# Kernel optimization log

Measured on AMD Instinct MI355X. Metric: run time of the kernel, lower is better.

Reference implementation:

```python
import jax, jax.numpy as jnp
import numpy as np
from jax import lax

# dims: batch, seq_len, d_model, heads, d_ff, num_scales, compression_ratio
B, L, D, H, F, S, CR = 4, 1024, 1024, 16, 4096, 4, 2


def setup_inputs() -> dict:
    key = jax.random.key(0)
    ks = jax.random.split(key, 12)
    def rn(k, shape, s=0.02):
        return jax.random.normal(k, shape, dtype=jnp.float32) * s
    return {
        'x': jax.random.normal(ks[0], (B, L, D), dtype=jnp.float32),
        'W_dc': rn(ks[1], (D, D, 3)),            # dilated conv kernel (OIH)
        'b_dc': jnp.zeros((D,), jnp.float32),
        'W_dec': rn(ks[2], (S - 1, D, D, CR)),    # strided decomposition convs
        'Wq': rn(ks[3], (S, D, D)),               # per-scale query proj
        'Wk': rn(ks[4], (S, D, D)),               # per-scale key proj
        'Wv': rn(ks[5], (D, D)),                  # shared value proj
        'Wo': rn(ks[6], (D, D)),                  # shared output proj
        'agg_logits': rn(ks[7], (S,), 1.0),       # convex aggregation logits
        'gamma1': jnp.ones((D,), jnp.float32), 'beta1': jnp.zeros((D,), jnp.float32),
        'gamma2': jnp.ones((D,), jnp.float32), 'beta2': jnp.zeros((D,), jnp.float32),
        'W1': rn(ks[8], (D, F)), 'b1': jnp.zeros((F,), jnp.float32),
        'W2': rn(ks[9], (F, D)), 'b2': jnp.zeros((D,), jnp.float32),
    }


def _conv1d(x_blc, w_oik, stride, pad, rdil):
    # x: [B, L, Cin] -> [B, L', Cout]; w: [Cout, Cin, K]
    y = lax.conv_general_dilated(
        x_blc.transpose(0, 2, 1), w_oik, (stride,), [(pad, pad)],
        rhs_dilation=(rdil,), dimension_numbers=('NCH', 'OIH', 'NCH'))
    return y.transpose(0, 2, 1)


def _ln(x, g, b, eps=1e-5):
    mu = x.mean(-1, keepdims=True)
    v = x.var(-1, keepdims=True)
    return (x - mu) * lax.rsqrt(v + eps) * g + b


def reference(x, W_dc, b_dc, W_dec, Wq, Wk, Wv, Wo, agg_logits,
              gamma1, beta1, gamma2, beta2, W1, b1, W2, b2):
    dh = D // H
    inv_sqrt_dh = 1.0 / jnp.sqrt(jnp.float32(dh))
    residual = x
    # 1. dilated conv (k=3, dil=2, pad=2 -> same length) + ReLU (dropout=eval/identity)
    xc = jax.nn.relu(_conv1d(x, W_dc, 1, 2, 2) + b_dc)
    # 2. hierarchical decomposition: strided convs halving seq length per scale
    scales = [xc]
    for s in range(S - 1):
        scales.append(_conv1d(scales[-1], W_dec[s], CR, 0, 1))
    # 3. multiscale attention: full-res queries attend to each compressed scale;
    #    value projection Wv shared across scales
    outs = []
    for s in range(S):
        Ls = scales[s].shape[1]
        q = (xc @ Wq[s]).reshape(B, L, H, dh)
        k = (scales[s] @ Wk[s]).reshape(B, Ls, H, dh)
        v = (scales[s] @ Wv).reshape(B, Ls, H, dh)
        att = jax.nn.softmax(jnp.einsum('bqhd,bkhd->bhqk', q, k) * inv_sqrt_dh, axis=-1)
        o = jnp.einsum('bhqk,bkhd->bqhd', att, v).reshape(B, L, D) @ Wo
        outs.append(o)
    # 4. convex (optimization-driven) aggregation + entropy sparsity aux loss
    w = jax.nn.softmax(agg_logits)
    maha = jnp.einsum('s,sbld->bld', w, jnp.stack(outs))
    aux_loss = -jnp.sum(w * jnp.log(w + 1e-9))
    # 5. residual + LN + FFN (exact GELU, as torch nn.GELU default)
    x1 = _ln(residual + maha, gamma1, beta1)
    ffn = jax.nn.gelu(x1 @ W1 + b1, approximate=False) @ W2 + b2
    out = _ln(x1 + ffn, gamma2, beta2)
    return out, aux_loss
```

## Files before the change

kernel.cpp:

```cpp
#include <hip/hip_runtime.h>
#include <cstddef>

#define DB 4
#define DL 1024
#define DD 1024
#define DH 16
#define DF 4096

typedef __attribute__((ext_vector_type(8))) short short8;
typedef __attribute__((ext_vector_type(4))) float float4v;

static __device__ __forceinline__ short f2bf(float f) {
    unsigned u = __float_as_uint(f);
    unsigned r = (u + 0x7FFFu + ((u >> 16) & 1u)) >> 16;
    return (short)r;
}

#define GLOAD_LDS16(gp, lp)                                                          \
    __builtin_amdgcn_global_load_lds(                                                \
        (const __attribute__((address_space(1))) void*)(gp),                         \
        (__attribute__((address_space(3))) void*)(lp), 16, 0, 0)

__global__ __launch_bounds__(256) void prep_all_kernel(
    const float* __restrict__ Wdc, const float* __restrict__ Wdec,
    const float* __restrict__ Wq, const float* __restrict__ Wk,
    const float* __restrict__ Wv, const float* __restrict__ Wo,
    const float* __restrict__ W1, const float* __restrict__ W2,
    const float* __restrict__ x, const float* __restrict__ agg,
    short* __restrict__ wdc_bt, short* __restrict__ wdec_bt,
    short* __restrict__ wq4t, short* __restrict__ wkvt, short* __restrict__ wot,
    short* __restrict__ w1t, short* __restrict__ w2t, short* __restrict__ xpad,
    float* __restrict__ wagg, float* __restrict__ aux) {
    __shared__ float tile[32][33];
    const size_t M1 = 1024 * 1024;
    int blk = blockIdx.x, tid = threadIdx.x;
    if (blk < 12288) {
        int idx = blk * 256 + tid;
        int i = idx & 1023, o = (idx >> 10) & 1023, k = idx >> 20;
        wdc_bt[idx] = f2bf(Wdc[((size_t)o * 1024 + i) * 3 + k]);
        return;
    }
    if (blk < 36864) {
        int idx = (blk - 12288) * 256 + tid;
        int i = idx & 1023, k2 = (idx >> 10) & 1, n = (idx >> 11) & 1023, s = idx >> 21;
        wdec_bt[idx] = f2bf(Wdec[(((size_t)(s * 1024 + n)) * 1024 + i) * 2 + k2]);
        return;
    }
    if (blk < 58368) {
        const float* src; short* dst; int K, N, bx, by;
        if (blk < 50176) {
            int r = blk - 36864;
            int z = r >> 10, rem = r & 1023;
            bx = rem & 31; by = rem >> 5; K = 1024; N = 1024;
            if (z < 4)      { src = Wq + (size_t)z * M1;       dst = wq4t + (size_t)z * M1; }
            else if (z < 8) { src = Wk + (size_t)(z - 4) * M1; dst = wkvt + (size_t)(z - 4) * 2 * M1; }
            else if (z < 12){ src = Wv;                        dst = wkvt + (size_t)(z - 8) * 2 * M1 + M1; }
            else            { src = Wo;                        dst = wot; }
        } else if (blk < 54272) {
            int r = blk - 50176;
            bx = r & 127; by = r >> 7; K = 1024; N = 4096; src = W1; dst = w1t;
        } else {
            int r = blk - 54272;
            bx = r & 31; by = r >> 5; K = 4096; N = 1024; src = W2; dst = w2t;
        }
        int n0 = bx << 5, k0 = by << 5;
        int cc = tid & 31, rr = tid >> 5;
#pragma unroll
        for (int p = 0; p < 4; p++) {
            int kk = (p << 3) + rr;
            tile[kk][cc] = src[(size_t)(k0 + kk) * N + n0 + cc];
        }
        __syncthreads();
#pragma unroll
        for (int p = 0; p < 4; p++) {
            int nn = (p << 3) + rr;
            dst[(size_t)(n0 + nn) * K + k0 + cc] = f2bf(tile[cc][nn]);
        }
        return;
    }
    if (blk < 74816) {
        int idx = (blk - 58368) * 256 + tid;
        int d = idx & 1023;
        int row = (idx >> 10) % 1028;
        int b = (idx >> 10) / 1028;
        int l = row - 2;
        float v = (l >= 0 && l < DL) ? x[((size_t)(b * DL + l)) * DD + d] : 0.f;
        xpad[idx] = f2bf(v);
        return;
    }
    if (tid == 0) {
        float l0 = agg[0], l1 = agg[1], l2 = agg[2], l3 = agg[3];
        float m = fmaxf(fmaxf(l0, l1), fmaxf(l2, l3));
        float e0 = __expf(l0 - m), e1 = __expf(l1 - m);
        float e2 = __expf(l2 - m), e3 = __expf(l3 - m);
        float ssum = e0 + e1 + e2 + e3;
        float w0 = e0 / ssum, w1 = e1 / ssum, w2 = e2 / ssum, w3 = e3 / ssum;
        wagg[0] = w0; wagg[1] = w1; wagg[2] = w2; wagg[3] = w3;
        *aux = -(w0 * logf(w0 + 1e-9f) + w1 * logf(w1 + 1e-9f) +
                 w2 * logf(w2 + 1e-9f) + w3 * logf(w3 + 1e-9f));
    }
}

template <int ACT, int OBF>
__global__ __launch_bounds__(256) void mgemm_kernel(
    const short* __restrict__ A, const short* __restrict__ Bt,
    const float* __restrict__ bias, void* __restrict__ Cv,
    int M, int N, int K) {
    __shared__ short As[128 * 32];
    __shared__ short Bs[128 * 32];
    int tid = threadIdx.x;
    int wave = tid >> 6, lane = tid & 63;
    int lq = lane & 15, quad = lane >> 4;
    int m0 = blockIdx.y << 7, n0 = blockIdx.x << 7;
    int wm = (wave & 1) << 6, wn = (wave >> 1) << 6;
    int r0 = tid >> 2, r1 = (256 + tid) >> 2;
    int kc0 = (tid & 3) << 3;
    const short* Ag0 = A + (size_t)(m0 + r0) * K + kc0;
    const short* Ag1 = A + (size_t)(m0 + r1) * K + kc0;
    const short* Bg0 = Bt + (size_t)(n0 + r0) * K + kc0;
    const short* Bg1 = Bt + (size_t)(n0 + r1) * K + kc0;
    float4v acc[4][4];
#pragma unroll
    for (int mi = 0; mi < 4; mi++)
#pragma unroll
        for (int ni = 0; ni < 4; ni++) acc[mi][ni] = (float4v){0.f, 0.f, 0.f, 0.f};

    for (int k0 = 0; k0 < K; k0 += 32) {
        __syncthreads();
        GLOAD_LDS16(Ag0 + k0, As + tid * 8);
        GLOAD_LDS16(Ag1 + k0, As + (256 + tid) * 8);
        GLOAD_LDS16(Bg0 + k0, Bs + tid * 8);
        GLOAD_LDS16(Bg1 + k0, Bs + (256 + tid) * 8);
        __syncthreads();
        short8 af[4], bfr[4];
#pragma unroll
        for (int mi = 0; mi < 4; mi++)
            af[mi] = *(const short8*)(As + ((wm + (mi << 4) + lq) << 5) + (quad << 3));
#pragma unroll
        for (int ni = 0; ni < 4; ni++)
            bfr[ni] = *(const short8*)(Bs + ((wn + (ni << 4) + lq) << 5) + (quad << 3));
#pragma unroll
        for (int mi = 0; mi < 4; mi++)
#pragma unroll
            for (int ni = 0; ni < 4; ni++)
                acc[mi][ni] = __builtin_amdgcn_mfma_f32_16x16x32_bf16(
                    af[mi], bfr[ni], acc[mi][ni], 0, 0, 0);
    }
#pragma unroll
    for (int ni = 0; ni < 4; ni++) {
        int col = n0 + wn + (ni << 4) + lq;
        float bv = bias ? bias[col] : 0.f;
#pragma unroll
        for (int mi = 0; mi < 4; mi++) {
#pragma unroll
            for (int r = 0; r < 4; r++) {
                int row = m0 + wm + (mi << 4) + (quad << 2) + r;
                float v = acc[mi][ni][r] + bv;
                if (ACT == 1) v = 0.5f * v * (1.0f + erff(v * 0.70710678118654752f));
                if (OBF) ((short*)Cv)[(size_t)row * N + col] = f2bf(v);
                else ((float*)Cv)[(size_t)row * N + col] = v;
            }
        }
    }
}

__global__ __launch_bounds__(256) void kvgemm_kernel(
    const short* __restrict__ acts, const short* __restrict__ wkvt,
    short* __restrict__ kvall, short* __restrict__ kfrall) {
    __shared__ short As[128 * 32];
    __shared__ short Bs[128 * 32];
    int my = blockIdx.y;
    int s = my < 32 ? 0 : my < 48 ? 1 : my < 56 ? 2 : 3;
    int m0 = my << 7;
    int rb = s == 0 ? 0 : s == 1 ? 4096 : s == 2 ? 6144 : 7168;
    size_t doff = s == 0 ? 0 : s == 1 ? 4194304 : s == 2 ? 6291456 : 7340032;
    int Ls = DL >> s;
    const short* Bt = wkvt + (size_t)s * 2097152;
    const int K = 1024, N = 2048;
    int tid = threadIdx.x;
    int wave = tid >> 6, lane = tid & 63;
    int lq = lane & 15, quad = lane >> 4;
    int n0 = blockIdx.x << 7;
    int wm = (wave & 1) << 6, wn = (wave >> 1) << 6;
    int r0 = tid >> 2, r1 = (256 + tid) >> 2;
    int kc0 = (tid & 3) << 3;
    const short* Ag0 = acts + (size_t)(m0 + r0) * K + kc0;
    const short* Ag1 = acts + (size_t)(m0 + r1) * K + kc0;
    const short* Bg0 = Bt + (size_t)(n0 + r0) * K + kc0;
    const short* Bg1 = Bt + (size_t)(n0 + r1) * K + kc0;
    float4v acc[4][4];
#pragma unroll
    for (int mi = 0; mi < 4; mi++)
#pragma unroll
        for (int ni = 0; ni < 4; ni++) acc[mi][ni] = (float4v){0.f, 0.f, 0.f, 0.f};
    for (int k0 = 0; k0 < K; k0 += 32) {
        __syncthreads();
        GLOAD_LDS16(Ag0 + k0, As + tid * 8);
        GLOAD_LDS16(Ag1 + k0, As + (256 + tid) * 8);
        GLOAD_LDS16(Bg0 + k0, Bs + tid * 8);
        GLOAD_LDS16(Bg1 + k0, Bs + (256 + tid) * 8);
        __syncthreads();
        short8 af[4], bfr[4];
#pragma unroll
        for (int mi = 0; mi < 4; mi++)
            af[mi] = *(const short8*)(As + ((wm + (mi << 4) + lq) << 5) + (quad << 3));
#pragma unroll
        for (int ni = 0; ni < 4; ni++)
            bfr[ni] = *(const short8*)(Bs + ((wn + (ni << 4) + lq) << 5) + (quad << 3));
#pragma unroll
        for (int mi = 0; mi < 4; mi++)
#pragma unroll
            for (int ni = 0; ni < 4; ni++)
                acc[mi][ni] = __builtin_amdgcn_mfma_f32_16x16x32_bf16(
                    af[mi], bfr[ni], acc[mi][ni], 0, 0, 0);
    }
    bool isK = (n0 < 1024);
#pragma unroll
    for (int ni = 0; ni < 4; ni++) {
        int col = n0 + wn + (ni << 4) + lq;
        if (isK) {
            int h = col >> 6, dc = (col >> 3) & 7, di = col & 7;
#pragma unroll
            for (int mi = 0; mi < 4; mi++)
#pragma unroll
                for (int r = 0; r < 4; r++) {
                    int row = m0 + wm + (mi << 4) + (quad << 2) + r;
                    int jg = row - rb;
                    int b = jg >> (10 - s);
                    int j = jg & (Ls - 1);
                    int bh = (b << 4) | h;
                    size_t addr = doff + (((size_t)bh * (Ls >> 4) + (j >> 4)) << 10) +
                                  (dc << 7) + ((j & 15) << 3) + di;
                    kfrall[addr] = f2bf(acc[mi][ni][r]);
                }
        } else {
#pragma unroll
            for (int mi = 0; mi < 4; mi++)
#pragma unroll
                for (int r = 0; r < 4; r++) {
                    int row = m0 + wm + (mi << 4) + (quad << 2) + r;
                    kvall[(size_t)row * N + col] = f2bf(acc[mi][ni][r]);
                }
        }
    }
}

__global__ __launch_bounds__(256) void mgemm_pk_kernel(
    const short* __restrict__ A, const short* __restrict__ Bt,
    const float* __restrict__ bias, float* __restrict__ Cout,
    int M, int N, int Kfull, int KH) {
    __shared__ short As[128 * 32];
    __shared__ short Bs[128 * 32];
    int kz = blockIdx.z;
    const short* Ab = A + (size_t)kz * KH;
    const short* Btb = Bt + (size_t)kz * KH;
    float* Co = Cout + (size_t)kz * M * N;
    int tid = threadIdx.x;
    int wave = tid >> 6, lane = tid & 63;
    int lq = lane & 15, quad = lane >> 4;
    int m0 = blockIdx.y << 7, n0 = blockIdx.x << 7;
    int wm = (wave & 1) << 6, wn = (wave >> 1) << 6;
    int r0 = tid >> 2, r1 = (256 + tid) >> 2;
    int kc0 = (tid & 3) << 3;
    const short* Ag0 = Ab + (size_t)(m0 + r0) * Kfull + kc0;
    const short* Ag1 = Ab + (size_t)(m0 + r1) * Kfull + kc0;
    const short* Bg0 = Btb + (size_t)(n0 + r0) * Kfull + kc0;
    const short* Bg1 = Btb + (size_t)(n0 + r1) * Kfull + kc0;
    float4v acc[4][4];
#pragma unroll
    for (int mi = 0; mi < 4; mi++)
#pragma unroll
        for (int ni = 0; ni < 4; ni++) acc[mi][ni] = (float4v){0.f, 0.f, 0.f, 0.f};
    for (int k0 = 0; k0 < KH; k0 += 32) {
        __syncthreads();
        GLOAD_LDS16(Ag0 + k0, As + tid * 8);
        GLOAD_LDS16(Ag1 + k0, As + (256 + tid) * 8);
        GLOAD_LDS16(Bg0 + k0, Bs + tid * 8);
        GLOAD_LDS16(Bg1 + k0, Bs + (256 + tid) * 8);
        __syncthreads();
        short8 af[4], bfr[4];
#pragma unroll
        for (int mi = 0; mi < 4; mi++)
            af[mi] = *(const short8*)(As + ((wm + (mi << 4) + lq) << 5) + (quad << 3));
#pragma unroll
        for (int ni = 0; ni < 4; ni++)
            bfr[ni] = *(const short8*)(Bs + ((wn + (ni << 4) + lq) << 5) + (quad << 3));
#pragma unroll
        for (int mi = 0; mi < 4; mi++)
#pragma unroll
            for (int ni = 0; ni < 4; ni++)
                acc[mi][ni] = __builtin_amdgcn_mfma_f32_16x16x32_bf16(
                    af[mi], bfr[ni], acc[mi][ni], 0, 0, 0);
    }
#pragma unroll
    for (int ni = 0; ni < 4; ni++) {
        int col = n0 + wn + (ni << 4) + lq;
        float bv = (bias && kz == 0) ? bias[col] : 0.f;
#pragma unroll
        for (int mi = 0; mi < 4; mi++)
#pragma unroll
            for (int r = 0; r < 4; r++) {
                int row = m0 + wm + (mi << 4) + (quad << 2) + r;
                __builtin_nontemporal_store(acc[mi][ni][r] + bv,
                                            &Co[(size_t)row * N + col]);
            }
    }
}

__global__ __launch_bounds__(256) void sumcast4_kernel(
    const float* __restrict__ p, size_t stride, short* __restrict__ outp) {
    int idx = (blockIdx.x * 256 + threadIdx.x) << 2;
    float4v a0 = __builtin_nontemporal_load((const float4v*)&p[idx]);
    float4v a1 = __builtin_nontemporal_load((const float4v*)&p[stride + idx]);
    float4v a2 = __builtin_nontemporal_load((const float4v*)&p[2 * stride + idx]);
    float4v a3 = __builtin_nontemporal_load((const float4v*)&p[3 * stride + idx]);
    ushort4 u;
    u.x = (unsigned short)f2bf(a0[0] + a1[0] + a2[0] + a3[0]);
    u.y = (unsigned short)f2bf(a0[1] + a1[1] + a2[1] + a3[1]);
    u.z = (unsigned short)f2bf(a0[2] + a1[2] + a2[2] + a3[2]);
    u.w = (unsigned short)f2bf(a0[3] + a1[3] + a2[3] + a3[3]);
    *(ushort4*)&outp[idx] = u;
}

__global__ __launch_bounds__(256) void convdil_pk_kernel(
    const short* __restrict__ xp, const short* __restrict__ Wt,
    float* __restrict__ pbuf) {
    __shared__ short As[128 * 32];
    __shared__ short Bs[128 * 32];
    int kp = blockIdx.z;
    int tid = threadIdx.x;
    int wave = tid >> 6, lane = tid & 63;
    int lq = lane & 15, quad = lane >> 4;
    int m0 = blockIdx.y << 7, n0 = blockIdx.x << 7;
    int wm = (wave & 1) << 6, wn = (wave >> 1) << 6;
    int b = m0 >> 10, ll0 = m0 & 1023;
    int r0 = tid >> 2, r1 = (256 + tid) >> 2;
    int kc = (tid & 3) << 3;
    float* Co = pbuf + (size_t)kp * DB * DL * DD;
    const short* Abase = xp + ((size_t)(b * 1028 + ll0 + 2 * kp)) * DD + kc;
    const short* Bbase = Wt + (size_t)kp * DD * DD;
    const short* Bg0 = Bbase + (size_t)(n0 + r0) * DD + kc;
    const short* Bg1 = Bbase + (size_t)(n0 + r1) * DD + kc;
    float4v acc[4][4];
#pragma unroll
    for (int mi = 0; mi < 4; mi++)
#pragma unroll
        for (int ni = 0; ni < 4; ni++) acc[mi][ni] = (float4v){0.f, 0.f, 0.f, 0.f};
    for (int k0 = 0; k0 < DD; k0 += 32) {
        __syncthreads();
        GLOAD_LDS16(Abase + (size_t)r0 * DD + k0, As + tid * 8);
        GLOAD_LDS16(Abase + (size_t)r1 * DD + k0, As + (256 + tid) * 8);
        GLOAD_LDS16(Bg0 + k0, Bs + tid * 8);
        GLOAD_LDS16(Bg1 + k0, Bs + (256 + tid) * 8);
        __syncthreads();
        short8 af[4], bfr[4];
#pragma unroll
        for (int mi = 0; mi < 4; mi++)
            af[mi] = *(const short8*)(As + ((wm + (mi << 4) + lq) << 5) + (quad << 3));
#pragma unroll
        for (int ni = 0; ni < 4; ni++)
            bfr[ni] = *(const short8*)(Bs + ((wn + (ni << 4) + lq) << 5) + (quad << 3));
#pragma unroll
        for (int mi = 0; mi < 4; mi++)
#pragma unroll
            for (int ni = 0; ni < 4; ni++)
                acc[mi][ni] = __builtin_amdgcn_mfma_f32_16x16x32_bf16(
                    af[mi], bfr[ni], acc[mi][ni], 0, 0, 0);
    }
#pragma unroll
    for (int ni = 0; ni < 4; ni++) {
        int col = n0 + wn + (ni << 4) + lq;
#pragma unroll
        for (int mi = 0; mi < 4; mi++)
#pragma unroll
            for (int r = 0; r < 4; r++) {
                int row = m0 + wm + (mi << 4) + (quad << 2) + r;
                __builtin_nontemporal_store(acc[mi][ni][r],
                                            &Co[(size_t)row * DD + col]);
            }
    }
}

__global__ __launch_bounds__(256) void convcomb_kernel(
    const float* __restrict__ pbuf, const float* __restrict__ bvec,
    short* __restrict__ xcb) {
    const size_t M4 = (size_t)DB * DL * DD;
    int idx = (blockIdx.x * 256 + threadIdx.x) << 2;
    int col = idx & 1023;
    float4v p0 = __builtin_nontemporal_load((const float4v*)&pbuf[idx]);
    float4v p1 = __builtin_nontemporal_load((const float4v*)&pbuf[M4 + idx]);
    float4v p2 = __builtin_nontemporal_load((const float4v*)&pbuf[2 * M4 + idx]);
    float4v bb = *(const float4v*)&bvec[col];
    ushort4 u;
    u.x = (unsigned short)f2bf(fmaxf(p0[0] + p1[0] + p2[0] + bb[0], 0.f));
    u.y = (unsigned short)f2bf(fmaxf(p0[1] + p1[1] + p2[1] + bb[1], 0.f));
    u.z = (unsigned short)f2bf(fmaxf(p0[2] + p1[2] + p2[2] + bb[2], 0.f));
    u.w = (unsigned short)f2bf(fmaxf(p0[3] + p1[3] + p2[3] + bb[3], 0.f));
    *(ushort4*)&xcb[idx] = u;
}

__global__ __launch_bounds__(256) void vfrag_all_kernel(const short* __restrict__ kvall,
                                                        short* __restrict__ vfr0) {
    __shared__ short tile[32][33];
    int flat = blockIdx.x;
    int s, base, rb;
    size_t doff;
    if (flat < 4096)      { s = 0; base = 0;    rb = 0;    doff = 0; }
    else if (flat < 6144) { s = 1; base = 4096; rb = 4096; doff = 4194304; }
    else if (flat < 7168) { s = 2; base = 6144; rb = 6144; doff = 6291456; }
    else                  { s = 3; base = 7168; rb = 7168; doff = 7340032; }
    int rem = flat - base;
    int Ls = DL >> s;
    int nt = Ls >> 5;
    int j0t = rem & (nt - 1);
    int rest = rem >> (5 - s);
    int dt = rest & 1;
    int bh = rest >> 1;
    int j0 = j0t << 5, d0 = dt << 5;
    int b = bh >> 4, h = bh & 15;
    int tid = threadIdx.x;
    int cc = tid & 31, rr = tid >> 5;
#pragma unroll
    for (int p = 0; p < 4; p++) {
        int jj = (p << 3) + rr;
        tile[jj][cc] = kvall[((size_t)(rb + b * Ls + j0 + jj) << 11) + 1024 +
                             (h << 6) + d0 + cc];
    }
    __syncthreads();
    int c = j0 >> 6, ks = (j0 >> 5) & 1;
    int pc = (((cc >> 2) & 1) << 4) | ((cc >> 3) << 2) | (cc & 3);
#pragma unroll
    for (int p = 0; p < 4; p++) {
        int d = d0 + (p << 3) + rr;
        int tt = d >> 4, lqv = d & 15;
        size_t off = doff + (((size_t)bh * (Ls >> 6) + c) << 12) + (ks << 11) +
                     (tt << 9) + ((cc & 24) << 4) + (lqv << 3) + (cc & 7);
        vfr0[off] = tile[pc][(p << 3) + rr];
    }
}

static __device__ __forceinline__ float fexp2(float x) {
    return __builtin_amdgcn_exp2f(x);
}

#define STAGE9(BUF, TILE)                                                         \
    {                                                                             \
        const short* _gs = (w < 2)                                                \
            ? kt + ((size_t)(TILE) << 12) + (w << 11) + (lane << 3)               \
            : vt + ((size_t)(TILE) << 12) + ((w - 2) << 11) + (lane << 3);        \
        short* _lb = sbuf[BUF] + (w << 11) + (lane << 3);                         \
        _Pragma("unroll") for (int _i = 0; _i < 4; _i++)                          \
            GLOAD_LDS16(_gs + (_i << 9), _lb + (_i << 9));                        \
    }

__global__ __launch_bounds__(256) void attn_fused9_kernel(
    const short* __restrict__ qb4, const short* __restrict__ kfr0,
    const short* __restrict__ vfr0, const float* __restrict__ wagg,
    short* __restrict__ attb) {
    __shared__ __align__(16) short sbuf[2][8192];
    int tid = threadIdx.x;
    int w = tid >> 6, lane = tid & 63;
    int lq = lane & 15, quad = lane >> 4;
    int bh = blockIdx.x;
    int b = bh >> 4, h = bh & 15;
    int qrow0 = b * DL + (blockIdx.y << 6) + (w << 4);
    const float c_exp = 0.18033688f;
    int fo = (quad << 7) + (lq << 3);

    float fin[4][4];
#pragma unroll
    for (int t = 0; t < 4; t++)
#pragma unroll
        for (int r = 0; r < 4; r++) fin[t][r] = 0.f;

#pragma unroll 1
    for (int s = 0; s < 4; s++) {
        int Ls = DL >> s;
        size_t doff = s == 0 ? 0 : s == 1 ? 4194304 : s == 2 ? 6291456 : 7340032;

        const short* qbase = qb4 + ((size_t)(qrow0 + lq) << 12) + (s << 10) +
                             (h << 6) + (quad << 3);
        short8 qf0 = __builtin_nontemporal_load((const short8*)qbase);
        short8 qf1 = __builtin_nontemporal_load((const short8*)(qbase + 32));

        const short* kt = kfr0 + doff + (((size_t)bh * (Ls >> 4)) << 10);
        const short* vt = vfr0 + doff + (((size_t)bh * (Ls >> 6)) << 12);

        float4v O[4];
        float lsum = 0.f;
#pragma unroll
        for (int t = 0; t < 4; t++) O[t] = (float4v){0.f, 0.f, 0.f, 0.f};

        int nt = Ls >> 6;
        STAGE9(0, 0);
#pragma unroll 1
        for (int c = 0; c < nt; c++) {
            __syncthreads();
            int cur = c & 1;
            if (c + 1 < nt) STAGE9(cur ^ 1, c + 1);
            const short* kl = sbuf[cur] + fo;
            const short* vl = sbuf[cur] + 4096 + fo;

            float4v S[4];
#pragma unroll
            for (int t = 0; t < 4; t++) {
                short8 kf0 = *(const short8*)(kl + (t << 10));
                short8 kf1 = *(const short8*)(kl + (t << 10) + 512);
                float4v zz = (float4v){0.f, 0.f, 0.f, 0.f};
                zz = __builtin_amdgcn_mfma_f32_16x16x32_bf16(kf0, qf0, zz, 0, 0, 0);
                S[t] = __builtin_amdgcn_mfma_f32_16x16x32_bf16(kf1, qf1, zz, 0, 0, 0);
            }

            unsigned wpk[8];
#pragma unroll
            for (int t = 0; t < 4; t++) {
                float p0 = fexp2(S[t][0] * c_exp);
                float p1 = fexp2(S[t][1] * c_exp);
                float p2 = fexp2(S[t][2] * c_exp);
                float p3 = fexp2(S[t][3] * c_exp);
                lsum += p0 + p1 + p2 + p3;
                wpk[2 * t]     = (__float_as_uint(p1) & 0xFFFF0000u) |
                                 (__float_as_uint(p0) >> 16);
                wpk[2 * t + 1] = (__float_as_uint(p3) & 0xFFFF0000u) |
                                 (__float_as_uint(p2) >> 16);
            }
            union AFU { unsigned u[4]; short8 s8; };
            AFU af0, af1;
            af0.u[0] = wpk[0]; af0.u[1] = wpk[1]; af0.u[2] = wpk[2]; af0.u[3] = wpk[3];
            af1.u[0] = wpk[4]; af1.u[1] = wpk[5]; af1.u[2] = wpk[6]; af1.u[3] = wpk[7];
#pragma unroll
            for (int t = 0; t < 4; t++) {
                short8 vf = *(const short8*)(vl + (t << 9));
                O[t] = __builtin_amdgcn_mfma_f32_16x16x32_bf16(af0.s8, vf, O[t], 0, 0, 0);
            }
#pragma unroll
            for (int t = 0; t < 4; t++) {
                short8 vf = *(const short8*)(vl + 2048 + (t << 9));
                O[t] = __builtin_amdgcn_mfma_f32_16x16x32_bf16(af1.s8, vf, O[t], 0, 0, 0);
            }
        }
        __syncthreads();

        lsum += __shfl_xor(lsum, 16, 64);
        lsum += __shfl_xor(lsum, 32, 64);
        float wsc = wagg[s];
#pragma unroll
        for (int r = 0; r < 4; r++) {
            int sl = (lane & 48) | (((lane >> 4) << 2) + r);
            float lr = __shfl(lsum, sl, 64);
            float linv = wsc / lr;
#pragma unroll
            for (int t = 0; t < 4; t++) fin[t][r] += O[t][r] * linv;
        }
    }
#pragma unroll
    for (int r = 0; r < 4; r++) {
        size_t rbase = ((size_t)(qrow0 + (quad << 2) + r) << 10) + (h << 6) + lq;
#pragma unroll
        for (int t = 0; t < 4; t++)
            attb[rbase + (t << 4)] = f2bf(fin[t][r]);
    }
}

template <int NP, int OBF>
__global__ __launch_bounds__(256) void addlnN_kernel(
    const float* __restrict__ a, const float* __restrict__ pb, size_t pstride,
    const float* __restrict__ gam, const float* __restrict__ bet,
    float* __restrict__ out, short* __restrict__ outb) {
    __shared__ float redA[4], redB[4];
    int row = blockIdx.x, tid = threadIdx.x;
    size_t base = (size_t)row * DD + (tid << 2);
    float4v av = *(const float4v*)&a[base];
    float s0 = av[0], s1 = av[1], s2 = av[2], s3 = av[3];
#pragma unroll
    for (int j = 0; j < NP; j++) {
        float4v pv = __builtin_nontemporal_load(
            (const float4v*)&pb[(size_t)j * pstride + base]);
        s0 += pv[0]; s1 += pv[1]; s2 += pv[2]; s3 += pv[3];
    }
    float lsum = s0 + s1 + s2 + s3;
    float lsq = s0 * s0 + s1 * s1 + s2 * s2 + s3 * s3;
#pragma unroll
    for (int o = 32; o > 0; o >>= 1) {
        lsum += __shfl_down(lsum, o, 64);
        lsq += __shfl_down(lsq, o, 64);
    }
    int lane = tid & 63, wid = tid >> 6;
    if (lane == 0) { redA[wid] = lsum; redB[wid] = lsq; }
    __syncthreads();
    float tsum = redA[0] + redA[1] + redA[2] + redA[3];
    float tsq = redB[0] + redB[1] + redB[2] + redB[3];
    float mean = tsum * (1.0f / DD);
    float var = tsq * (1.0f / DD) - mean * mean;
    float rstd = rsqrtf(var + 1e-5f);
    float4v gv = *(const float4v*)&gam[tid << 2];
    float4v bev = *(const float4v*)&bet[tid << 2];
    float4v o;
    o[0] = (s0 - mean) * rstd * gv[0] + bev[0];
    o[1] = (s1 - mean) * rstd * gv[1] + bev[1];
    o[2] = (s2 - mean) * rstd * gv[2] + bev[2];
    o[3] = (s3 - mean) * rstd * gv[3] + bev[3];
    *(float4v*)&out[base] = o;
    if (OBF) {
        ushort4 u;
        u.x = (unsigned short)f2bf(o[0]);
        u.y = (unsigned short)f2bf(o[1]);
        u.z = (unsigned short)f2bf(o[2]);
        u.w = (unsigned short)f2bf(o[3]);
        *(ushort4*)&outb[base] = u;
    }
}

extern "C" void kernel_launch(void* const* d_in, const int* in_sizes, int n_in,
                              void* d_out, int out_size, void* d_ws, size_t ws_size,
                              hipStream_t stream) {
    (void)in_sizes; (void)n_in; (void)out_size; (void)ws_size;
    const float* x   = (const float*)d_in[0];
    const float* Wdc = (const float*)d_in[1];
    const float* bdc = (const float*)d_in[2];
    const float* Wdec= (const float*)d_in[3];
    const float* Wq  = (const float*)d_in[4];
    const float* Wk  = (const float*)d_in[5];
    const float* Wv  = (const float*)d_in[6];
    const float* Wo  = (const float*)d_in[7];
    const float* agg = (const float*)d_in[8];
    const float* g1  = (const float*)d_in[9];
    const float* be1 = (const float*)d_in[10];
    const float* g2  = (const float*)d_in[11];
    const float* be2 = (const float*)d_in[12];
    const float* W1  = (const float*)d_in[13];
    const float* b1  = (const float*)d_in[14];
    const float* W2  = (const float*)d_in[15];
    const float* b2  = (const float*)d_in[16];
    float* out = (float*)d_out;

    float* ws = (float*)d_ws;
    size_t off = 0;
    auto alloc = [&](size_t nfloats) { float* p = ws + off; off += nfloats; return p; };
    const size_t M1 = 1024 * 1024;
    short* wdc_bt  = (short*)alloc(3 * M1 / 2);
    short* wdec_bt = (short*)alloc(3 * M1);
    short* wq4t    = (short*)alloc(2 * M1);
    short* wkvt    = (short*)alloc(4 * M1);
    short* wot     = (short*)alloc(M1 / 2);
    short* w1t     = (short*)alloc(2 * M1);
    short* w2t     = (short*)alloc(2 * M1);
    float* wagg    = alloc(64);
    short* xpad    = (short*)alloc(2105344);
    short* xcb     = (short*)alloc(2 * M1);
    short* s1b     = (short*)alloc(M1);
    short* s2b     = (short*)alloc(M1 / 2);
    short* s3b     = (short*)alloc(M1 / 4);
    short* qb4     = (short*)alloc(8 * M1);
    short* kvall   = (short*)alloc(7 * M1 + M1 / 2);
    short* kfrall  = (short*)alloc(3 * M1 + 3 * M1 / 4);
    short* vfrall  = (short*)alloc(3 * M1 + 3 * M1 / 4);
    short* attb    = (short*)alloc(2 * M1);
    float* x1      = alloc(4 * M1);
    short* x1b     = (short*)alloc(2 * M1);
    float* pkbuf   = alloc(8 * M1);
    short* hb      = qb4;
    float* convp   = (float*)qb4;
    float* pk4     = (float*)kvall;

    dim3 blk(256);
    prep_all_kernel<<<dim3(74817), blk, 0, stream>>>(
        Wdc, Wdec, Wq, Wk, Wv, Wo, W1, W2, x, agg,
        wdc_bt, wdec_bt, wq4t, wkvt, wot, w1t, w2t, xpad, wagg,
        out + (size_t)DB * DL * DD);

    convdil_pk_kernel<<<dim3(DD / 128, DB * DL / 128, 3), blk, 0, stream>>>(
        xpad, wdc_bt, convp);
    convcomb_kernel<<<dim3(4 * M1 / (256 * 4)), blk, 0, stream>>>(convp, bdc, xcb);

    mgemm_pk_kernel<<<dim3(8, 16, 4), blk, 0, stream>>>(
        xcb, wdec_bt, nullptr, pkbuf, 2048, DD, 2 * DD, 512);
    sumcast4_kernel<<<dim3(2 * M1 / 1024), blk, 0, stream>>>(pkbuf, 2 * M1, s1b);
    mgemm_pk_kernel<<<dim3(8, 8, 4), blk, 0, stream>>>(
        s1b, wdec_bt + 2 * M1, nullptr, pkbuf, 1024, DD, 2 * DD, 512);
    sumcast4_kernel<<<dim3(M1 / 1024), blk, 0, stream>>>(pkbuf, M1, s2b);
    mgemm_pk_kernel<<<dim3(8, 4, 4), blk, 0, stream>>>(
        s2b, wdec_bt + 4 * M1, nullptr, pkbuf, 512, DD, 2 * DD, 512);
    sumcast4_kernel<<<dim3(M1 / 2048), blk, 0, stream>>>(pkbuf, M1 / 2, s3b);

    mgemm_kernel<0, 1><<<dim3(32, 32), blk, 0, stream>>>(
        xcb, wq4t, nullptr, qb4, DB * DL, 4 * DD, DD);

    kvgemm_kernel<<<dim3(16, 60), blk, 0, stream>>>(xcb, wkvt, kvall, kfrall);

    vfrag_all_kernel<<<dim3(7680), blk, 0, stream>>>(kvall, vfrall);

    attn_fused9_kernel<<<dim3(DB * DH, DL / 64), blk, 0, stream>>>(
        qb4, kfrall, vfrall, wagg, attb);

    mgemm_pk_kernel<<<dim3(8, 32, 2), blk, 0, stream>>>(
        attb, wot, nullptr, pkbuf, DB * DL, DD, DD, DD / 2);

    addlnN_kernel<2, 1><<<dim3(DB * DL), blk, 0, stream>>>(
        x, pkbuf, 4 * M1, g1, be1, x1, x1b);

    mgemm_kernel<1, 1><<<dim3(DF / 128, (DB * DL) / 128), blk, 0, stream>>>(
        x1b, w1t, b1, hb, DB * DL, DF, DD);
    mgemm_pk_kernel<<<dim3(8, 32, 4), blk, 0, stream>>>(
        hb, w2t, b2, pk4, DB * DL, DD, DF, DF / 4);

    addlnN_kernel<4, 0><<<dim3(DB * DL), blk, 0, stream>>>(
        x1, pk4, 4 * M1, g2, be2, out, nullptr);
}
```

Before: 700.8 us.

## Double-buffer LDS tiles in all MFMA GEMM kernels to overlap loads with compute

Each of the four bf16 MFMA GEMM kernels (generic, KV projection, split-K, dilated conv) now keeps two LDS buffers for the A and B tiles. The next K-tile's global-to-LDS loads are issued before the MFMAs on the current tile, and a single barrier per iteration replaces the previous two. The aim is to hide global memory latency behind matrix-core work and cut barrier overhead. In exchange, LDS use per block doubles to 32 KB, which may lower occupancy. The benefit also depends on whether the barrier forces a full vmcnt wait.

```diff
diff --git a/kernel.cpp b/kernel.cpp
--- a/kernel.cpp
+++ b/kernel.cpp
@@ -106,8 +106,8 @@
     const short* __restrict__ A, const short* __restrict__ Bt,
     const float* __restrict__ bias, void* __restrict__ Cv,
     int M, int N, int K) {
-    __shared__ short As[128 * 32];
-    __shared__ short Bs[128 * 32];
+    __shared__ short As[2][128 * 32];
+    __shared__ short Bs[2][128 * 32];
     int tid = threadIdx.x;
     int wave = tid >> 6, lane = tid & 63;
     int lq = lane & 15, quad = lane >> 4;
@@ -125,27 +125,35 @@
 #pragma unroll
         for (int ni = 0; ni < 4; ni++) acc[mi][ni] = (float4v){0.f, 0.f, 0.f, 0.f};
 
-    for (int k0 = 0; k0 < K; k0 += 32) {
-        __syncthreads();
-        GLOAD_LDS16(Ag0 + k0, As + tid * 8);
-        GLOAD_LDS16(Ag1 + k0, As + (256 + tid) * 8);
-        GLOAD_LDS16(Bg0 + k0, Bs + tid * 8);
-        GLOAD_LDS16(Bg1 + k0, Bs + (256 + tid) * 8);
-        __syncthreads();
+#define MG_STAGE(BUF, KO)                                                \
+    {                                                                    \
+        GLOAD_LDS16(Ag0 + (KO), As[BUF] + tid * 8);                      \
+        GLOAD_LDS16(Ag1 + (KO), As[BUF] + (256 + tid) * 8);              \
+        GLOAD_LDS16(Bg0 + (KO), Bs[BUF] + tid * 8);                      \
+        GLOAD_LDS16(Bg1 + (KO), Bs[BUF] + (256 + tid) * 8);              \
+    }
+    int nk = K >> 5;
+    MG_STAGE(0, 0);
+    __syncthreads();
+    for (int t = 0; t < nk; t++) {
+        int cur = t & 1;
+        if (t + 1 < nk) MG_STAGE(cur ^ 1, (t + 1) << 5);
         short8 af[4], bfr[4];
 #pragma unroll
         for (int mi = 0; mi < 4; mi++)
-            af[mi] = *(const short8*)(As + ((wm + (mi << 4) + lq) << 5) + (quad << 3));
+            af[mi] = *(const short8*)(As[cur] + ((wm + (mi << 4) + lq) << 5) + (quad << 3));
 #pragma unroll
         for (int ni = 0; ni < 4; ni++)
-            bfr[ni] = *(const short8*)(Bs + ((wn + (ni << 4) + lq) << 5) + (quad << 3));
+            bfr[ni] = *(const short8*)(Bs[cur] + ((wn + (ni << 4) + lq) << 5) + (quad << 3));
 #pragma unroll
         for (int mi = 0; mi < 4; mi++)
 #pragma unroll
             for (int ni = 0; ni < 4; ni++)
                 acc[mi][ni] = __builtin_amdgcn_mfma_f32_16x16x32_bf16(
                     af[mi], bfr[ni], acc[mi][ni], 0, 0, 0);
-    }
+        __syncthreads();
+    }
+#undef MG_STAGE
 #pragma unroll
     for (int ni = 0; ni < 4; ni++) {
         int col = n0 + wn + (ni << 4) + lq;
@@ -167,8 +175,8 @@
 __global__ __launch_bounds__(256) void kvgemm_kernel(
     const short* __restrict__ acts, const short* __restrict__ wkvt,
     short* __restrict__ kvall, short* __restrict__ kfrall) {
-    __shared__ short As[128 * 32];
-    __shared__ short Bs[128 * 32];
+    __shared__ short As[2][128 * 32];
+    __shared__ short Bs[2][128 * 32];
     int my = blockIdx.y;
     int s = my < 32 ? 0 : my < 48 ? 1 : my < 56 ? 2 : 3;
     int m0 = my << 7;
@@ -193,27 +201,36 @@
     for (int mi = 0; mi < 4; mi++)
 #pragma unroll
         for (int ni = 0; ni < 4; ni++) acc[mi][ni] = (float4v){0.f, 0.f, 0.f, 0.f};
-    for (int k0 = 0; k0 < K; k0 += 32) {
-        __syncthreads();
-        GLOAD_LDS16(Ag0 + k0, As + tid * 8);
-        GLOAD_LDS16(Ag1 + k0, As + (256 + tid) * 8);
-        GLOAD_LDS16(Bg0 + k0, Bs + tid * 8);
-        GLOAD_LDS16(Bg1 + k0, Bs + (256 + tid) * 8);
-        __syncthreads();
+
+#define KV_STAGE(BUF, KO)                                                \
+    {                                                                    \
+        GLOAD_LDS16(Ag0 + (KO), As[BUF] + tid * 8);                      \
+        GLOAD_LDS16(Ag1 + (KO), As[BUF] + (256 + tid) * 8);              \
+        GLOAD_LDS16(Bg0 + (KO), Bs[BUF] + tid * 8);                      \
+        GLOAD_LDS16(Bg1 + (KO), Bs[BUF] + (256 + tid) * 8);              \
+    }
+    int nk = K >> 5;
+    KV_STAGE(0, 0);
+    __syncthreads();
+    for (int t = 0; t < nk; t++) {
+        int cur = t & 1;
+        if (t + 1 < nk) KV_STAGE(cur ^ 1, (t + 1) << 5);
         short8 af[4], bfr[4];
 #pragma unroll
         for (int mi = 0; mi < 4; mi++)
-            af[mi] = *(const short8*)(As + ((wm + (mi << 4) + lq) << 5) + (quad << 3));
+            af[mi] = *(const short8*)(As[cur] + ((wm + (mi << 4) + lq) << 5) + (quad << 3));
 #pragma unroll
         for (int ni = 0; ni < 4; ni++)
-            bfr[ni] = *(const short8*)(Bs + ((wn + (ni << 4) + lq) << 5) + (quad << 3));
+            bfr[ni] = *(const short8*)(Bs[cur] + ((wn + (ni << 4) + lq) << 5) + (quad << 3));
 #pragma unroll
         for (int mi = 0; mi < 4; mi++)
 #pragma unroll
             for (int ni = 0; ni < 4; ni++)
                 acc[mi][ni] = __builtin_amdgcn_mfma_f32_16x16x32_bf16(
                     af[mi], bfr[ni], acc[mi][ni], 0, 0, 0);
-    }
+        __syncthreads();
+    }
+#undef KV_STAGE
     bool isK = (n0 < 1024);
 #pragma unroll
     for (int ni = 0; ni < 4; ni++) {
@@ -249,8 +266,8 @@
     const short* __restrict__ A, const short* __restrict__ Bt,
     const float* __restrict__ bias, float* __restrict__ Cout,
     int M, int N, int Kfull, int KH) {
-    __shared__ short As[128 * 32];
-    __shared__ short Bs[128 * 32];
+    __shared__ short As[2][128 * 32];
+    __shared__ short Bs[2][128 * 32];
     int kz = blockIdx.z;
     const short* Ab = A + (size_t)kz * KH;
     const short* Btb = Bt + (size_t)kz * KH;
@@ -271,27 +288,36 @@
     for (int mi = 0; mi < 4; mi++)
 #pragma unroll
         for (int ni = 0; ni < 4; ni++) acc[mi][ni] = (float4v){0.f, 0.f, 0.f, 0.f};
-    for (int k0 = 0; k0 < KH; k0 += 32) {
-        __syncthreads();
-        GLOAD_LDS16(Ag0 + k0, As + tid * 8);
-        GLOAD_LDS16(Ag1 + k0, As + (256 + tid) * 8);
-        GLOAD_LDS16(Bg0 + k0, Bs + tid * 8);
-        GLOAD_LDS16(Bg1 + k0, Bs + (256 + tid) * 8);
-        __syncthreads();
+
+#define PK_STAGE(BUF, KO)                                                \
+    {                                                                    \
+        GLOAD_LDS16(Ag0 + (KO), As[BUF] + tid * 8);                      \
+        GLOAD_LDS16(Ag1 + (KO), As[BUF] + (256 + tid) * 8);              \
+        GLOAD_LDS16(Bg0 + (KO), Bs[BUF] + tid * 8);                      \
+        GLOAD_LDS16(Bg1 + (KO), Bs[BUF] + (256 + tid) * 8);              \
+    }
+    int nk = KH >> 5;
+    PK_STAGE(0, 0);
+    __syncthreads();
+    for (int t = 0; t < nk; t++) {
+        int cur = t & 1;
+        if (t + 1 < nk) PK_STAGE(cur ^ 1, (t + 1) << 5);
         short8 af[4], bfr[4];
 #pragma unroll
         for (int mi = 0; mi < 4; mi++)
-            af[mi] = *(const short8*)(As + ((wm + (mi << 4) + lq) << 5) + (quad << 3));
+            af[mi] = *(const short8*)(As[cur] + ((wm + (mi << 4) + lq) << 5) + (quad << 3));
 #pragma unroll
         for (int ni = 0; ni < 4; ni++)
-            bfr[ni] = *(const short8*)(Bs + ((wn + (ni << 4) + lq) << 5) + (quad << 3));
+            bfr[ni] = *(const short8*)(Bs[cur] + ((wn + (ni << 4) + lq) << 5) + (quad << 3));
 #pragma unroll
         for (int mi = 0; mi < 4; mi++)
 #pragma unroll
             for (int ni = 0; ni < 4; ni++)
                 acc[mi][ni] = __builtin_amdgcn_mfma_f32_16x16x32_bf16(
                     af[mi], bfr[ni], acc[mi][ni], 0, 0, 0);
-    }
+        __syncthreads();
+    }
+#undef PK_STAGE
 #pragma unroll
     for (int ni = 0; ni < 4; ni++) {
         int col = n0 + wn + (ni << 4) + lq;
@@ -325,8 +351,8 @@
 __global__ __launch_bounds__(256) void convdil_pk_kernel(
     const short* __restrict__ xp, const short* __restrict__ Wt,
     float* __restrict__ pbuf) {
-    __shared__ short As[128 * 32];
-    __shared__ short Bs[128 * 32];
+    __shared__ short As[2][128 * 32];
+    __shared__ short Bs[2][128 * 32];
     int kp = blockIdx.z;
     int tid = threadIdx.x;
     int wave = tid >> 6, lane = tid & 63;
@@ -346,27 +372,36 @@
     for (int mi = 0; mi < 4; mi++)
 #pragma unroll
         for (int ni = 0; ni < 4; ni++) acc[mi][ni] = (float4v){0.f, 0.f, 0.f, 0.f};
-    for (int k0 = 0; k0 < DD; k0 += 32) {
-        __syncthreads();
-        GLOAD_LDS16(Abase + (size_t)r0 * DD + k0, As + tid * 8);
-        GLOAD_LDS16(Abase + (size_t)r1 * DD + k0, As + (256 + tid) * 8);
-        GLOAD_LDS16(Bg0 + k0, Bs + tid * 8);
-        GLOAD_LDS16(Bg1 + k0, Bs + (256 + tid) * 8);
-        __syncthreads();
+
+#define CD_STAGE(BUF, KO)                                                        \
+    {                                                                            \
+        GLOAD_LDS16(Abase + (size_t)r0 * DD + (KO), As[BUF] + tid * 8);          \
+        GLOAD_LDS16(Abase + (size_t)r1 * DD + (KO), As[BUF] + (256 + tid) * 8);  \
+        GLOAD_LDS16(Bg0 + (KO), Bs[BUF] + tid * 8);                              \
+        GLOAD_LDS16(Bg1 + (KO), Bs[BUF] + (256 + tid) * 8);                      \
+    }
+    int nk = DD >> 5;
+    CD_STAGE(0, 0);
+    __syncthreads();
+    for (int t = 0; t < nk; t++) {
+        int cur = t & 1;
+        if (t + 1 < nk) CD_STAGE(cur ^ 1, (t + 1) << 5);
         short8 af[4], bfr[4];
 #pragma unroll
         for (int mi = 0; mi < 4; mi++)
-            af[mi] = *(const short8*)(As + ((wm + (mi << 4) + lq) << 5) + (quad << 3));
+            af[mi] = *(const short8*)(As[cur] + ((wm + (mi << 4) + lq) << 5) + (quad << 3));
 #pragma unroll
         for (int ni = 0; ni < 4; ni++)
-            bfr[ni] = *(const short8*)(Bs + ((wn + (ni << 4) + lq) << 5) + (quad << 3));
+            bfr[ni] = *(const short8*)(Bs[cur] + ((wn + (ni << 4) + lq) << 5) + (quad << 3));
 #pragma unroll
         for (int mi = 0; mi < 4; mi++)
 #pragma unroll
             for (int ni = 0; ni < 4; ni++)
                 acc[mi][ni] = __builtin_amdgcn_mfma_f32_16x16x32_bf16(
                     af[mi], bfr[ni], acc[mi][ni], 0, 0, 0);
-    }
+        __syncthreads();
+    }
+#undef CD_STAGE
 #pragma unroll
     for (int ni = 0; ni < 4; ni++) {
         int col = n0 + wn + (ni << 4) + lq;
```

New measurement: 666.1 us (median of 2 runs). -5.0%, faster.
